# Kernel optimization log

Hardware: AMD Instinct MI355X
Metric: run time of the kernel (lower is better)

Reference implementation:

```python
import jax, jax.numpy as jnp
import numpy as np

EMBED, HEADS, LEVELS, POINTS = 256, 8, 3, 4
SPATIAL = np.array([[128, 128], [64, 64], [32, 32]], dtype=np.int64)  # (H, W) per level
B = 2
S = int((SPATIAL[:, 0] * SPATIAL[:, 1]).sum())  # 21504
Q = S  # encoder self-attention: queries == flattened multi-scale features


def grid_sample_bilinear(img, grid):
    """img: [N,C,H,W]; grid: [N,Q,P,2] (x,y) in [-1,1]; bilinear, zeros padding, align_corners=False.
    Returns [N,C,Q,P]."""
    N, C, H, W = img.shape
    _, Qn, Pn, _ = grid.shape
    x = (grid[..., 0] + 1.0) * (W * 0.5) - 0.5
    y = (grid[..., 1] + 1.0) * (H * 0.5) - 0.5
    x0 = jnp.floor(x)
    y0 = jnp.floor(y)
    wx1 = x - x0
    wy1 = y - y0
    x0i = x0.astype(jnp.int32)
    y0i = y0.astype(jnp.int32)
    imgf = img.reshape(N, C, H * W)

    def gather(ix, iy):
        valid = (ix >= 0) & (ix < W) & (iy >= 0) & (iy < H)
        ixc = jnp.clip(ix, 0, W - 1)
        iyc = jnp.clip(iy, 0, H - 1)
        flat = (iyc * W + ixc).reshape(N, -1)  # [N, Q*P]
        v = jax.vmap(lambda im, f: im[:, f])(imgf, flat)  # [N, C, Q*P]
        return jnp.where(valid.reshape(N, 1, -1), v, 0.0)

    w00 = ((1.0 - wx1) * (1.0 - wy1)).reshape(N, 1, -1)
    w01 = (wx1 * (1.0 - wy1)).reshape(N, 1, -1)
    w10 = ((1.0 - wx1) * wy1).reshape(N, 1, -1)
    w11 = (wx1 * wy1).reshape(N, 1, -1)
    out = (gather(x0i, y0i) * w00 + gather(x0i + 1, y0i) * w01
           + gather(x0i, y0i + 1) * w10 + gather(x0i + 1, y0i + 1) * w11)
    return out.reshape(N, C, Qn, Pn)


def msda_forward(hidden_states, encoder_hidden_states, reference_points, shapes_np,
                 sampling_offsets_w, sampling_offsets_b, attention_weights_w, attention_weights_b,
                 value_proj_w, value_proj_b, output_proj_w, output_proj_b):
    Bn, Qn, E = hidden_states.shape
    H, L, P = HEADS, LEVELS, POINTS
    D = E // H
    Sn = encoder_hidden_states.shape[1]
    value = (encoder_hidden_states @ value_proj_w.T + value_proj_b).reshape(Bn, Sn, H, D)
    off = (hidden_states @ sampling_offsets_w.T + sampling_offsets_b).reshape(Bn, Qn, H, L, P, 2)
    aw = hidden_states @ attention_weights_w.T + attention_weights_b
    aw = jax.nn.softmax(aw.reshape(Bn, Qn, H, L * P), axis=-1).reshape(Bn, Qn, H, L, P)
    # offset normalizer is (W, H) per level
    norm = jnp.asarray(np.stack([shapes_np[:, 1], shapes_np[:, 0]], axis=-1), dtype=hidden_states.dtype)
    loc = reference_points[:, :, None, :, None, :] + off / norm[None, None, None, :, None, :]
    grids = 2.0 * loc - 1.0  # [B,Q,H,L,P,2]
    out = jnp.zeros((Bn * H, D, Qn), value.dtype)
    start = 0
    for lvl in range(L):  # small static loop over levels (distinct spatial shapes)
        h, w = int(shapes_np[lvl, 0]), int(shapes_np[lvl, 1])
        val_l = value[:, start:start + h * w].transpose(0, 2, 3, 1).reshape(Bn * H, D, h, w)
        start += h * w
        g = grids[:, :, :, lvl].transpose(0, 2, 1, 3, 4).reshape(Bn * H, Qn, P, 2)
        sampled = grid_sample_bilinear(val_l, g)  # [B*H, D, Q, P]
        w_l = aw[:, :, :, lvl].transpose(0, 2, 1, 3).reshape(Bn * H, 1, Qn, P)
        out = out + (sampled * w_l).sum(-1)
    out = out.reshape(Bn, H * D, Qn).transpose(0, 2, 1)  # [B,Q,E]
    return out @ output_proj_w.T + output_proj_b


def setup_inputs():
    key = jax.random.key(0)
    ks = jax.random.split(key, 11)
    sc = 0.02
    E, H, L, P = EMBED, HEADS, LEVELS, POINTS
    return {
        "hidden_states": jax.random.normal(ks[0], (B, Q, E), jnp.float32),
        "encoder_hidden_states": jax.random.normal(ks[1], (B, S, E), jnp.float32),
        "reference_points": jax.random.uniform(ks[2], (B, Q, L, 2), jnp.float32),
        "spatial_shapes": jnp.asarray(SPATIAL),
        "sampling_offsets_w": jax.random.normal(ks[3], (H * L * P * 2, E), jnp.float32) * sc,
        "sampling_offsets_b": jax.random.normal(ks[4], (H * L * P * 2,), jnp.float32) * sc,
        "attention_weights_w": jax.random.normal(ks[5], (H * L * P, E), jnp.float32) * sc,
        "attention_weights_b": jax.random.normal(ks[6], (H * L * P,), jnp.float32) * sc,
        "value_proj_w": jax.random.normal(ks[7], (E, E), jnp.float32) * sc,
        "value_proj_b": jax.random.normal(ks[8], (E,), jnp.float32) * sc,
        "output_proj_w": jax.random.normal(ks[9], (E, E), jnp.float32) * sc,
        "output_proj_b": jax.random.normal(ks[10], (E,), jnp.float32) * sc,
    }


def reference(hidden_states, encoder_hidden_states, reference_points, spatial_shapes,
              sampling_offsets_w, sampling_offsets_b, attention_weights_w, attention_weights_b,
              value_proj_w, value_proj_b, output_proj_w, output_proj_b):
    shapes_np = np.asarray(spatial_shapes)  # static per-level (H, W)
    return msda_forward(hidden_states, encoder_hidden_states, reference_points, shapes_np,
                        sampling_offsets_w, sampling_offsets_b, attention_weights_w, attention_weights_b,
                        value_proj_w, value_proj_b, output_proj_w, output_proj_b)
```

## Files before the change

### kernel.cpp

```cpp
#include <hip/hip_runtime.h>
#include <hip/hip_bf16.h>

#define EMBED   256
#define HEADS   8
#define LEVELS  3
#define POINTS  4
#define BATCH   2
#define QLEN    21504
#define SLEN    21504
#define MTOT    (BATCH * QLEN)

typedef __attribute__((ext_vector_type(8))) short short8;
typedef __attribute__((ext_vector_type(4))) float f32x4;
typedef __attribute__((ext_vector_type(2))) float f32x2;

__device__ __forceinline__ short f2bf(float x) {
    unsigned u = __builtin_bit_cast(unsigned, x);
    u += 0x7fffu + ((u >> 16) & 1u);
    return (short)(u >> 16);
}
__device__ __forceinline__ f32x2 bfpair(unsigned u) {
    f32x2 r;
    r.x = __builtin_bit_cast(float, u << 16);
    r.y = __builtin_bit_cast(float, u & 0xffff0000u);
    return r;
}

__global__ __launch_bounds__(256)
void pack_weights_kernel(const float* __restrict__ vW, const float* __restrict__ oW,
                         const float* __restrict__ soW, const float* __restrict__ awW,
                         const float* __restrict__ soB, const float* __restrict__ awB,
                         short* __restrict__ vWf, short* __restrict__ oWf,
                         short* __restrict__ soawWf, float* __restrict__ soawB)
{
    int i = blockIdx.x * 256 + threadIdx.x;
    if (i < 25600) {
        const float* src; short* dst; int rem;
        if (i < 8192)       { src = vW; dst = vWf; rem = i; }
        else if (i < 16384) { src = oW; dst = oWf; rem = i - 8192; }
        else                { src = nullptr; dst = soawWf; rem = i - 16384; }
        const int lane = rem & 63;
        const int kt   = (rem >> 6) & 7;
        const int ct   = rem >> 9;
        const int col  = ct * 16 + (lane & 15);
        const int kb   = (kt * 4 + (lane >> 4)) * 8;
        const float* p = src ? (src + col * 256 + kb)
                             : ((col < 192) ? (soW + col * 256 + kb)
                                            : (awW + (col - 192) * 256 + kb));
        short8 t;
        #pragma unroll
        for (int j = 0; j < 8; ++j) t[j] = f2bf(p[j]);
        *(short8*)(dst + (size_t)rem * 8) = t;
    } else if (i < 25888) {
        int row = i - 25600;
        soawB[row] = (row < 192) ? soB[row] : awB[row - 192];
    }
}


__global__ __launch_bounds__(64, 4)
void proj_gemm_kernel(const float* __restrict__ enc, const short* __restrict__ vWf,
                      const float* __restrict__ vB, short* __restrict__ valb,
                      const float* __restrict__ hs, const short* __restrict__ soawWf,
                      const float* __restrict__ soawB, float* __restrict__ offaw)
{
    const int lane = threadIdx.x;
    const int m16  = lane & 15, ko = lane >> 4;
    const bool isVal = (blockIdx.x == 0);
    const float* A   = isVal ? enc : hs;
    const int strip  = blockIdx.y * 16;

    short8 afr[8];
    const float* Af = A + (size_t)(strip + m16) * 256 + ko * 8;
    #pragma unroll
    for (int kt = 0; kt < 8; ++kt) {
        float4 x = *(const float4*)(Af + kt * 32);
        float4 y = *(const float4*)(Af + kt * 32 + 4);
        short8 t;
        t[0] = f2bf(x.x); t[1] = f2bf(x.y); t[2] = f2bf(x.z); t[3] = f2bf(x.w);
        t[4] = f2bf(y.x); t[5] = f2bf(y.y); t[6] = f2bf(y.z); t[7] = f2bf(y.w);
        afr[kt] = t;
    }

    const short8* Wf  = (const short8*)(isVal ? vWf : soawWf);
    const float* bias = isVal ? vB : soawB;
    const int nct     = isVal ? 16 : 18;
    const int r0      = strip + ko * 4;

    for (int ct = 0; ct < nct; ++ct) {
        f32x4 a0 = (f32x4)0.f;
        #pragma unroll
        for (int kt = 0; kt < 8; ++kt) {
            const short8 bfrag = Wf[(ct * 8 + kt) * 64 + lane];
            a0 = __builtin_amdgcn_mfma_f32_16x16x32_bf16(afr[kt], bfrag, a0, 0, 0, 0);
        }
        const int col = ct * 16 + m16;
        const float bv = bias[col];
        if (isVal) {
            const int hh = col >> 5, ch = col & 31;
            #pragma unroll
            for (int r = 0; r < 4; ++r) {
                const int rg = r0 + r;
                const int b  = (rg >= SLEN) ? 1 : 0;
                const int sx = rg - b * SLEN;
                valb[(((size_t)(b * 8 + hh)) * SLEN + sx) * 32 + ch] = f2bf(a0[r] + bv);
            }
        } else {
            #pragma unroll
            for (int r = 0; r < 4; ++r)
                offaw[(size_t)(r0 + r) * 288 + col] = a0[r] + bv;
        }
    }
}

__global__ __launch_bounds__(64, 4)
void out_gemm_kernel(const short* __restrict__ A, const short* __restrict__ oWf,
                     const float* __restrict__ oB, float* __restrict__ C)
{
    const int lane = threadIdx.x;
    const int m16  = lane & 15, ko = lane >> 4;
    const int strip = blockIdx.x * 16;

    short8 afr[8];
    const short* Ab = A + (size_t)(strip + m16) * 256 + ko * 8;
    #pragma unroll
    for (int kt = 0; kt < 8; ++kt) afr[kt] = *(const short8*)(Ab + kt * 32);

    const short8* Wf = (const short8*)oWf;
    const int r0 = strip + ko * 4;
    for (int ct = 0; ct < 16; ++ct) {
        f32x4 a0 = (f32x4)0.f;
        #pragma unroll
        for (int kt = 0; kt < 8; ++kt) {
            const short8 bfrag = Wf[(ct * 8 + kt) * 64 + lane];
            a0 = __builtin_amdgcn_mfma_f32_16x16x32_bf16(afr[kt], bfrag, a0, 0, 0, 0);
        }
        const int col = ct * 16 + m16;
        const float bv = oB[col];
        #pragma unroll
        for (int r = 0; r < 4; ++r)
            C[(size_t)(r0 + r) * 256 + col] = a0[r] + bv;
    }
}

__global__ __launch_bounds__(256, 8)
void msda_sample_kernel(const short* __restrict__ value,
                        const float* __restrict__ offaw,
                        const float* __restrict__ ref,
                        short* __restrict__ attn)
{
    __shared__ int prep[32 * 76];

    const int tid = threadIdx.x;
    const int g   = tid >> 3;
    const int sub = tid & 7;
    const int t   = sub >> 2;

    const int blk = blockIdx.x;
    const int h   = blk & 7;
    const int j   = blk >> 3;
    const int b   = (j >= 672) ? 1 : 0;
    const int qc  = j - b * 672;
    const int q   = qc * 32 + g;
    const int bq  = b * QLEN + q;

    {
        const float* awp = offaw + (size_t)bq * 288 + 192 + h * 12;
        const float4 wa = *(const float4*)(awp);
        const float4 wb = *(const float4*)(awp + 4);
        const float4 wc = *(const float4*)(awp + 8);
        float w[12] = { wa.x, wa.y, wa.z, wa.w, wb.x, wb.y, wb.z, wb.w,
                        wc.x, wc.y, wc.z, wc.w };
        float mx = w[0];
        #pragma unroll
        for (int i = 1; i < 12; ++i) mx = fmaxf(mx, w[i]);
        float s = 0.f;
        #pragma unroll
        for (int i = 0; i < 12; ++i) s += __expf(w[i] - mx);
        const float inv = 1.f / s;

        const float* offp = offaw + (size_t)bq * 288 + h * 24;
        const float* refp = ref + (size_t)bq * 6;
        const int npts = (sub < 4) ? 2 : 1;
        #pragma unroll
        for (int it = 0; it < 2; ++it) {
            if (it >= npts) break;
            const int p  = sub + it * 8;
            const int l  = p >> 2;
            const int Wl = 128 >> l;
            const int st = (l == 0) ? 0 : (l == 1 ? 16384 : 20480);

            const float2 oxy = *(const float2*)(offp + p * 2);
            const float2 rxy = *(const float2*)(refp + 2 * l);
            const float ox = oxy.x, oy = oxy.y;
            const float rx = rxy.x, ry = rxy.y;
            const float a  = __expf(w[p] - mx) * inv;

            const float x = fmaf(rx, (float)Wl, ox - 0.5f);
            const float y = fmaf(ry, (float)Wl, oy - 0.5f);
            const float x0f = floorf(x), y0f = floorf(y);
            const int   x0  = (int)x0f,  y0  = (int)y0f;
            const float wx1 = x - x0f, wy1 = y - y0f;
            const float wx0 = 1.f - wx1, wy0 = 1.f - wy1;
            const bool vy0 = (unsigned)y0       < (unsigned)Wl;
            const bool vy1 = (unsigned)(y0 + 1) < (unsigned)Wl;

            const int xs = min(max(x0, 0), Wl - 2);
            const float wl0 = (xs == x0) ? wx0 : ((xs == x0 + 1) ? wx1 : 0.f);
            const float wl1 = (xs == x0) ? wx1 : ((xs + 1 == x0) ? wx0 : 0.f);

            const int hb = (b * 8 + h) * SLEN + st;
            const int o0 = vy0 ? (hb + y0 * Wl + xs) * 64       : 0;
            const int o1 = vy1 ? (hb + (y0 + 1) * Wl + xs) * 64 : 0;

            int* pp = &prep[g * 76 + p * 6];
            pp[0] = o0;
            pp[1] = o1;
            pp[2] = __builtin_bit_cast(int, vy0 ? wy0 * wl0 * a : 0.f);
            pp[3] = __builtin_bit_cast(int, vy0 ? wy0 * wl1 * a : 0.f);
            pp[4] = __builtin_bit_cast(int, vy1 ? wy1 * wl0 * a : 0.f);
            pp[5] = __builtin_bit_cast(int, vy1 ? wy1 * wl1 * a : 0.f);
        }
    }
    __syncthreads();

    const char* vbytes = (const char*)value;
    const unsigned subb = (unsigned)sub * 16u;
    f32x2 acc2[4];
    acc2[0] = (f32x2)0.f; acc2[1] = (f32x2)0.f;
    acc2[2] = (f32x2)0.f; acc2[3] = (f32x2)0.f;

    #pragma unroll
    for (int pb = 0; pb < 4; ++pb) {
        int4  v[6];
        float wgt[6];
        #pragma unroll
        for (int i = 0; i < 3; ++i) {
            const int p = pb * 3 + i;
            const int* pp = &prep[g * 76 + p * 6];
            const unsigned o0 = (unsigned)pp[0] + subb;
            const unsigned o1 = (unsigned)pp[1] + subb;
            wgt[2*i]   = __builtin_bit_cast(float, pp[2 + t]);
            wgt[2*i+1] = __builtin_bit_cast(float, pp[4 + t]);
            v[2*i]   = *(const int4*)(vbytes + (size_t)o0);
            v[2*i+1] = *(const int4*)(vbytes + (size_t)o1);
        }
        #pragma unroll
        for (int i = 0; i < 6; ++i) {
            f32x2 w2; w2.x = wgt[i]; w2.y = wgt[i];
            acc2[0] = __builtin_elementwise_fma(w2, bfpair((unsigned)v[i].x), acc2[0]);
            acc2[1] = __builtin_elementwise_fma(w2, bfpair((unsigned)v[i].y), acc2[1]);
            acc2[2] = __builtin_elementwise_fma(w2, bfpair((unsigned)v[i].z), acc2[2]);
            acc2[3] = __builtin_elementwise_fma(w2, bfpair((unsigned)v[i].w), acc2[3]);
        }
    }

    #pragma unroll
    for (int j2 = 0; j2 < 4; ++j2) {
        acc2[j2].x += __shfl_xor(acc2[j2].x, 4);
        acc2[j2].y += __shfl_xor(acc2[j2].y, 4);
    }

    if (sub < 4) {
        int4 o;
        o.x = ((unsigned)(unsigned short)f2bf(acc2[0].y) << 16) | (unsigned short)f2bf(acc2[0].x);
        o.y = ((unsigned)(unsigned short)f2bf(acc2[1].y) << 16) | (unsigned short)f2bf(acc2[1].x);
        o.z = ((unsigned)(unsigned short)f2bf(acc2[2].y) << 16) | (unsigned short)f2bf(acc2[2].x);
        o.w = ((unsigned)(unsigned short)f2bf(acc2[3].y) << 16) | (unsigned short)f2bf(acc2[3].x);
        ((int4*)attn)[(size_t)bq * 32 + h * 4 + sub] = o;
    }
}

extern "C" void kernel_launch(void* const* d_in, const int* in_sizes, int n_in,
                              void* d_out, int out_size, void* d_ws, size_t ws_size,
                              hipStream_t stream) {
    const float* hs  = (const float*)d_in[0];
    const float* enc = (const float*)d_in[1];
    const float* rp  = (const float*)d_in[2];
    const float* soW = (const float*)d_in[4];
    const float* soB = (const float*)d_in[5];
    const float* awW = (const float*)d_in[6];
    const float* awB = (const float*)d_in[7];
    const float* vW  = (const float*)d_in[8];
    const float* vB  = (const float*)d_in[9];
    const float* oW  = (const float*)d_in[10];
    const float* oB  = (const float*)d_in[11];
    float* out = (float*)d_out;

    const int M = MTOT;
    const size_t ME = (size_t)M * 256;

    short* valb   = (short*)d_ws;
    short* attnb  = valb + ME;
    float* offaw  = (float*)(attnb + ME);
    short* vWf    = (short*)(offaw + (size_t)M * 288);
    short* oWf    = vWf + 65536;
    short* soawWf = oWf + 65536;
    float* soawB  = (float*)(soawWf + 73728);

    pack_weights_kernel<<<dim3(102), dim3(256), 0, stream>>>(vW, oW, soW, awW, soB, awB,
                                                             vWf, oWf, soawWf, soawB);
    proj_gemm_kernel<<<dim3(2, M / 16), dim3(64), 0, stream>>>(enc, vWf, vB, valb,
                                                               hs, soawWf, soawB, offaw);
    msda_sample_kernel<<<dim3(M / 4), dim3(256), 0, stream>>>(valb, offaw, rp, attnb);
    out_gemm_kernel<<<dim3(M / 16), dim3(64), 0, stream>>>(attnb, oWf, oB, out);
}
```

Before: 270.2 us.

## Fuse all four stages into one persistent cooperative kernel with grid syncs

Merges the weight packing, projection GEMMs, deformable sampling and output GEMM into a single persistent cooperative kernel. The stages are separated by grid-wide syncs and work is spread with grid-stride loops over waves and blocks. The aim is to remove three kernel launch gaps and the tail effects between them. In exchange it adds grid barrier cost, caps the grid at 1024 blocks of 256 threads, and changes occupancy: the sampling stage moves from 8 to 4 blocks per CU and the GEMM stages from 64-thread blocks to 4 waves per block.

```diff
diff --git a/kernel.cpp b/kernel.cpp
--- a/kernel.cpp
+++ b/kernel.cpp
@@ -1,5 +1,8 @@
 #include <hip/hip_runtime.h>
 #include <hip/hip_bf16.h>
+#include <hip/hip_cooperative_groups.h>
+
+namespace cg = cooperative_groups;
 
 #define EMBED   256
 #define HEADS   8
@@ -26,248 +29,251 @@
     return r;
 }
 
-__global__ __launch_bounds__(256)
-void pack_weights_kernel(const float* __restrict__ vW, const float* __restrict__ oW,
-                         const float* __restrict__ soW, const float* __restrict__ awW,
-                         const float* __restrict__ soB, const float* __restrict__ awB,
-                         short* __restrict__ vWf, short* __restrict__ oWf,
-                         short* __restrict__ soawWf, float* __restrict__ soawB)
+__global__ __launch_bounds__(256, 4)
+void msda_fused(const float* __restrict__ hs, const float* __restrict__ enc,
+                const float* __restrict__ rp,
+                const float* __restrict__ soW, const float* __restrict__ soB,
+                const float* __restrict__ awW, const float* __restrict__ awB,
+                const float* __restrict__ vW,  const float* __restrict__ vB,
+                const float* __restrict__ oW,  const float* __restrict__ oB,
+                float* __restrict__ out,
+                short* __restrict__ valb, short* __restrict__ attnb,
+                float* __restrict__ offaw,
+                short* __restrict__ vWf, short* __restrict__ oWf,
+                short* __restrict__ soawWf, float* __restrict__ soawB)
 {
-    int i = blockIdx.x * 256 + threadIdx.x;
-    if (i < 25600) {
-        const float* src; short* dst; int rem;
-        if (i < 8192)       { src = vW; dst = vWf; rem = i; }
-        else if (i < 16384) { src = oW; dst = oWf; rem = i - 8192; }
-        else                { src = nullptr; dst = soawWf; rem = i - 16384; }
-        const int lane = rem & 63;
-        const int kt   = (rem >> 6) & 7;
-        const int ct   = rem >> 9;
-        const int col  = ct * 16 + (lane & 15);
-        const int kb   = (kt * 4 + (lane >> 4)) * 8;
-        const float* p = src ? (src + col * 256 + kb)
-                             : ((col < 192) ? (soW + col * 256 + kb)
-                                            : (awW + (col - 192) * 256 + kb));
-        short8 t;
-        #pragma unroll
-        for (int j = 0; j < 8; ++j) t[j] = f2bf(p[j]);
-        *(short8*)(dst + (size_t)rem * 8) = t;
-    } else if (i < 25888) {
-        int row = i - 25600;
-        soawB[row] = (row < 192) ? soB[row] : awB[row - 192];
-    }
-}
-
-
-__global__ __launch_bounds__(64, 4)
-void proj_gemm_kernel(const float* __restrict__ enc, const short* __restrict__ vWf,
-                      const float* __restrict__ vB, short* __restrict__ valb,
-                      const float* __restrict__ hs, const short* __restrict__ soawWf,
-                      const float* __restrict__ soawB, float* __restrict__ offaw)
-{
-    const int lane = threadIdx.x;
-    const int m16  = lane & 15, ko = lane >> 4;
-    const bool isVal = (blockIdx.x == 0);
-    const float* A   = isVal ? enc : hs;
-    const int strip  = blockIdx.y * 16;
-
-    short8 afr[8];
-    const float* Af = A + (size_t)(strip + m16) * 256 + ko * 8;
-    #pragma unroll
-    for (int kt = 0; kt < 8; ++kt) {
-        float4 x = *(const float4*)(Af + kt * 32);
-        float4 y = *(const float4*)(Af + kt * 32 + 4);
-        short8 t;
-        t[0] = f2bf(x.x); t[1] = f2bf(x.y); t[2] = f2bf(x.z); t[3] = f2bf(x.w);
-        t[4] = f2bf(y.x); t[5] = f2bf(y.y); t[6] = f2bf(y.z); t[7] = f2bf(y.w);
-        afr[kt] = t;
-    }
-
-    const short8* Wf  = (const short8*)(isVal ? vWf : soawWf);
-    const float* bias = isVal ? vB : soawB;
-    const int nct     = isVal ? 16 : 18;
-    const int r0      = strip + ko * 4;
-
-    for (int ct = 0; ct < nct; ++ct) {
-        f32x4 a0 = (f32x4)0.f;
+    __shared__ int prep[32 * 76];
+    cg::grid_group grid = cg::this_grid();
+
+    const int tid   = threadIdx.x;
+    const int nblk  = gridDim.x;
+    const int nwave = nblk * 4;
+    const int gwave = blockIdx.x * 4 + (tid >> 6);
+    const int lane  = tid & 63;
+    const int m16   = lane & 15, ko = lane >> 4;
+
+    for (int i = blockIdx.x * 256 + tid; i < 25888; i += nblk * 256) {
+        if (i < 25600) {
+            const float* src; short* dst; int rem;
+            if (i < 8192)       { src = vW; dst = vWf; rem = i; }
+            else if (i < 16384) { src = oW; dst = oWf; rem = i - 8192; }
+            else                { src = nullptr; dst = soawWf; rem = i - 16384; }
+            const int pl  = rem & 63;
+            const int kt  = (rem >> 6) & 7;
+            const int ct  = rem >> 9;
+            const int col = ct * 16 + (pl & 15);
+            const int kb  = (kt * 4 + (pl >> 4)) * 8;
+            const float* p = src ? (src + col * 256 + kb)
+                                 : ((col < 192) ? (soW + col * 256 + kb)
+                                                : (awW + (col - 192) * 256 + kb));
+            short8 t;
+            #pragma unroll
+            for (int j = 0; j < 8; ++j) t[j] = f2bf(p[j]);
+            *(short8*)(dst + (size_t)rem * 8) = t;
+        } else {
+            int row = i - 25600;
+            soawB[row] = (row < 192) ? soB[row] : awB[row - 192];
+        }
+    }
+    __threadfence();
+    grid.sync();
+
+    for (int u = gwave; u < 5376; u += nwave) {
+        const bool isVal = (u < 2688);
+        const int strip  = (isVal ? u : u - 2688) * 16;
+        const float* A   = isVal ? enc : hs;
+
+        short8 afr[8];
+        const float* Af = A + (size_t)(strip + m16) * 256 + ko * 8;
         #pragma unroll
         for (int kt = 0; kt < 8; ++kt) {
-            const short8 bfrag = Wf[(ct * 8 + kt) * 64 + lane];
-            a0 = __builtin_amdgcn_mfma_f32_16x16x32_bf16(afr[kt], bfrag, a0, 0, 0, 0);
-        }
-        const int col = ct * 16 + m16;
-        const float bv = bias[col];
-        if (isVal) {
-            const int hh = col >> 5, ch = col & 31;
-            #pragma unroll
-            for (int r = 0; r < 4; ++r) {
-                const int rg = r0 + r;
-                const int b  = (rg >= SLEN) ? 1 : 0;
-                const int sx = rg - b * SLEN;
-                valb[(((size_t)(b * 8 + hh)) * SLEN + sx) * 32 + ch] = f2bf(a0[r] + bv);
-            }
-        } else {
+            float4 x = *(const float4*)(Af + kt * 32);
+            float4 y = *(const float4*)(Af + kt * 32 + 4);
+            short8 t;
+            t[0] = f2bf(x.x); t[1] = f2bf(x.y); t[2] = f2bf(x.z); t[3] = f2bf(x.w);
+            t[4] = f2bf(y.x); t[5] = f2bf(y.y); t[6] = f2bf(y.z); t[7] = f2bf(y.w);
+            afr[kt] = t;
+        }
+
+        const short8* Wf  = (const short8*)(isVal ? vWf : soawWf);
+        const float* bias = isVal ? vB : soawB;
+        const int nct     = isVal ? 16 : 18;
+        const int r0      = strip + ko * 4;
+
+        for (int ct = 0; ct < nct; ++ct) {
+            f32x4 a0 = (f32x4)0.f;
+            #pragma unroll
+            for (int kt = 0; kt < 8; ++kt) {
+                const short8 bfrag = Wf[(ct * 8 + kt) * 64 + lane];
+                a0 = __builtin_amdgcn_mfma_f32_16x16x32_bf16(afr[kt], bfrag, a0, 0, 0, 0);
+            }
+            const int col = ct * 16 + m16;
+            const float bv = bias[col];
+            if (isVal) {
+                const int hh = col >> 5, ch = col & 31;
+                #pragma unroll
+                for (int r = 0; r < 4; ++r) {
+                    const int rg = r0 + r;
+                    const int b  = (rg >= SLEN) ? 1 : 0;
+                    const int sx = rg - b * SLEN;
+                    valb[(((size_t)(b * 8 + hh)) * SLEN + sx) * 32 + ch] = f2bf(a0[r] + bv);
+                }
+            } else {
+                #pragma unroll
+                for (int r = 0; r < 4; ++r)
+                    offaw[(size_t)(r0 + r) * 288 + col] = a0[r] + bv;
+            }
+        }
+    }
+    __threadfence();
+    grid.sync();
+
+    {
+        const int g   = tid >> 3;
+        const int sub = tid & 7;
+        const int t   = sub >> 2;
+
+        for (int u = blockIdx.x; u < 10752; u += nblk) {
+            const int h  = u & 7;
+            const int j  = u >> 3;
+            const int b  = (j >= 672) ? 1 : 0;
+            const int qc = j - b * 672;
+            const int q  = qc * 32 + g;
+            const int bq = b * QLEN + q;
+
+            {
+                const float* awp = offaw + (size_t)bq * 288 + 192 + h * 12;
+                const float4 wa = *(const float4*)(awp);
+                const float4 wb = *(const float4*)(awp + 4);
+                const float4 wc = *(const float4*)(awp + 8);
+                float w[12] = { wa.x, wa.y, wa.z, wa.w, wb.x, wb.y, wb.z, wb.w,
+                                wc.x, wc.y, wc.z, wc.w };
+                float mx = w[0];
+                #pragma unroll
+                for (int i = 1; i < 12; ++i) mx = fmaxf(mx, w[i]);
+                float s = 0.f;
+                #pragma unroll
+                for (int i = 0; i < 12; ++i) s += __expf(w[i] - mx);
+                const float inv = 1.f / s;
+
+                const float* offp = offaw + (size_t)bq * 288 + h * 24;
+                const float* refp = rp + (size_t)bq * 6;
+                const int npts = (sub < 4) ? 2 : 1;
+                #pragma unroll
+                for (int it = 0; it < 2; ++it) {
+                    if (it >= npts) break;
+                    const int p  = sub + it * 8;
+                    const int l  = p >> 2;
+                    const int Wl = 128 >> l;
+                    const int st = (l == 0) ? 0 : (l == 1 ? 16384 : 20480);
+
+                    const float2 oxy = *(const float2*)(offp + p * 2);
+                    const float2 rxy = *(const float2*)(refp + 2 * l);
+                    const float ox = oxy.x, oy = oxy.y;
+                    const float rx = rxy.x, ry = rxy.y;
+                    const float a  = __expf(w[p] - mx) * inv;
+
+                    const float x = fmaf(rx, (float)Wl, ox - 0.5f);
+                    const float y = fmaf(ry, (float)Wl, oy - 0.5f);
+                    const float x0f = floorf(x), y0f = floorf(y);
+                    const int   x0  = (int)x0f,  y0  = (int)y0f;
+                    const float wx1 = x - x0f, wy1 = y - y0f;
+                    const float wx0 = 1.f - wx1, wy0 = 1.f - wy1;
+                    const bool vy0 = (unsigned)y0       < (unsigned)Wl;
+                    const bool vy1 = (unsigned)(y0 + 1) < (unsigned)Wl;
+
+                    const int xs = min(max(x0, 0), Wl - 2);
+                    const float wl0 = (xs == x0) ? wx0 : ((xs == x0 + 1) ? wx1 : 0.f);
+                    const float wl1 = (xs == x0) ? wx1 : ((xs + 1 == x0) ? wx0 : 0.f);
+
+                    const int hb = (b * 8 + h) * SLEN + st;
+                    const int o0 = vy0 ? (hb + y0 * Wl + xs) * 64       : 0;
+                    const int o1 = vy1 ? (hb + (y0 + 1) * Wl + xs) * 64 : 0;
+
+                    int* pp = &prep[g * 76 + p * 6];
+                    pp[0] = o0;
+                    pp[1] = o1;
+                    pp[2] = __builtin_bit_cast(int, vy0 ? wy0 * wl0 * a : 0.f);
+                    pp[3] = __builtin_bit_cast(int, vy0 ? wy0 * wl1 * a : 0.f);
+                    pp[4] = __builtin_bit_cast(int, vy1 ? wy1 * wl0 * a : 0.f);
+                    pp[5] = __builtin_bit_cast(int, vy1 ? wy1 * wl1 * a : 0.f);
+                }
+            }
+            __syncthreads();
+
+            const char* vbytes = (const char*)valb;
+            const unsigned subb = (unsigned)sub * 16u;
+            f32x2 acc2[4];
+            acc2[0] = (f32x2)0.f; acc2[1] = (f32x2)0.f;
+            acc2[2] = (f32x2)0.f; acc2[3] = (f32x2)0.f;
+
+            #pragma unroll
+            for (int pb = 0; pb < 4; ++pb) {
+                int4  v[6];
+                float wgt[6];
+                #pragma unroll
+                for (int i = 0; i < 3; ++i) {
+                    const int p = pb * 3 + i;
+                    const int* pp = &prep[g * 76 + p * 6];
+                    const unsigned o0 = (unsigned)pp[0] + subb;
+                    const unsigned o1 = (unsigned)pp[1] + subb;
+                    wgt[2*i]   = __builtin_bit_cast(float, pp[2 + t]);
+                    wgt[2*i+1] = __builtin_bit_cast(float, pp[4 + t]);
+                    v[2*i]   = *(const int4*)(vbytes + (size_t)o0);
+                    v[2*i+1] = *(const int4*)(vbytes + (size_t)o1);
+                }
+                #pragma unroll
+                for (int i = 0; i < 6; ++i) {
+                    f32x2 w2; w2.x = wgt[i]; w2.y = wgt[i];
+                    acc2[0] = __builtin_elementwise_fma(w2, bfpair((unsigned)v[i].x), acc2[0]);
+                    acc2[1] = __builtin_elementwise_fma(w2, bfpair((unsigned)v[i].y), acc2[1]);
+                    acc2[2] = __builtin_elementwise_fma(w2, bfpair((unsigned)v[i].z), acc2[2]);
+                    acc2[3] = __builtin_elementwise_fma(w2, bfpair((unsigned)v[i].w), acc2[3]);
+                }
+            }
+
+            #pragma unroll
+            for (int j2 = 0; j2 < 4; ++j2) {
+                acc2[j2].x += __shfl_xor(acc2[j2].x, 4);
+                acc2[j2].y += __shfl_xor(acc2[j2].y, 4);
+            }
+
+            if (sub < 4) {
+                int4 o;
+                o.x = ((unsigned)(unsigned short)f2bf(acc2[0].y) << 16) | (unsigned short)f2bf(acc2[0].x);
+                o.y = ((unsigned)(unsigned short)f2bf(acc2[1].y) << 16) | (unsigned short)f2bf(acc2[1].x);
+                o.z = ((unsigned)(unsigned short)f2bf(acc2[2].y) << 16) | (unsigned short)f2bf(acc2[2].x);
+                o.w = ((unsigned)(unsigned short)f2bf(acc2[3].y) << 16) | (unsigned short)f2bf(acc2[3].x);
+                ((int4*)attnb)[(size_t)bq * 32 + h * 4 + sub] = o;
+            }
+            __syncthreads();
+        }
+    }
+    __threadfence();
+    grid.sync();
+
+    for (int u = gwave; u < 2688; u += nwave) {
+        const int strip = u * 16;
+        short8 afr[8];
+        const short* Ab = attnb + (size_t)(strip + m16) * 256 + ko * 8;
+        #pragma unroll
+        for (int kt = 0; kt < 8; ++kt) afr[kt] = *(const short8*)(Ab + kt * 32);
+
+        const short8* Wf = (const short8*)oWf;
+        const int r0 = strip + ko * 4;
+        for (int ct = 0; ct < 16; ++ct) {
+            f32x4 a0 = (f32x4)0.f;
+            #pragma unroll
+            for (int kt = 0; kt < 8; ++kt) {
+                const short8 bfrag = Wf[(ct * 8 + kt) * 64 + lane];
+                a0 = __builtin_amdgcn_mfma_f32_16x16x32_bf16(afr[kt], bfrag, a0, 0, 0, 0);
+            }
+            const int col = ct * 16 + m16;
+            const float bv = oB[col];
             #pragma unroll
             for (int r = 0; r < 4; ++r)
-                offaw[(size_t)(r0 + r) * 288 + col] = a0[r] + bv;
-        }
-    }
-}
-
-__global__ __launch_bounds__(64, 4)
-void out_gemm_kernel(const short* __restrict__ A, const short* __restrict__ oWf,
-                     const float* __restrict__ oB, float* __restrict__ C)
-{
-    const int lane = threadIdx.x;
-    const int m16  = lane & 15, ko = lane >> 4;
-    const int strip = blockIdx.x * 16;
-
-    short8 afr[8];
-    const short* Ab = A + (size_t)(strip + m16) * 256 + ko * 8;
-    #pragma unroll
-    for (int kt = 0; kt < 8; ++kt) afr[kt] = *(const short8*)(Ab + kt * 32);
-
-    const short8* Wf = (const short8*)oWf;
-    const int r0 = strip + ko * 4;
-    for (int ct = 0; ct < 16; ++ct) {
-        f32x4 a0 = (f32x4)0.f;
-        #pragma unroll
-        for (int kt = 0; kt < 8; ++kt) {
-            const short8 bfrag = Wf[(ct * 8 + kt) * 64 + lane];
-            a0 = __builtin_amdgcn_mfma_f32_16x16x32_bf16(afr[kt], bfrag, a0, 0, 0, 0);
-        }
-        const int col = ct * 16 + m16;
-        const float bv = oB[col];
-        #pragma unroll
-        for (int r = 0; r < 4; ++r)
-            C[(size_t)(r0 + r) * 256 + col] = a0[r] + bv;
-    }
-}
-
-__global__ __launch_bounds__(256, 8)
-void msda_sample_kernel(const short* __restrict__ value,
-                        const float* __restrict__ offaw,
-                        const float* __restrict__ ref,
-                        short* __restrict__ attn)
-{
-    __shared__ int prep[32 * 76];
-
-    const int tid = threadIdx.x;
-    const int g   = tid >> 3;
-    const int sub = tid & 7;
-    const int t   = sub >> 2;
-
-    const int blk = blockIdx.x;
-    const int h   = blk & 7;
-    const int j   = blk >> 3;
-    const int b   = (j >= 672) ? 1 : 0;
-    const int qc  = j - b * 672;
-    const int q   = qc * 32 + g;
-    const int bq  = b * QLEN + q;
-
-    {
-        const float* awp = offaw + (size_t)bq * 288 + 192 + h * 12;
-        const float4 wa = *(const float4*)(awp);
-        const float4 wb = *(const float4*)(awp + 4);
-        const float4 wc = *(const float4*)(awp + 8);
-        float w[12] = { wa.x, wa.y, wa.z, wa.w, wb.x, wb.y, wb.z, wb.w,
-                        wc.x, wc.y, wc.z, wc.w };
-        float mx = w[0];
-        #pragma unroll
-        for (int i = 1; i < 12; ++i) mx = fmaxf(mx, w[i]);
-        float s = 0.f;
-        #pragma unroll
-        for (int i = 0; i < 12; ++i) s += __expf(w[i] - mx);
-        const float inv = 1.f / s;
-
-        const float* offp = offaw + (size_t)bq * 288 + h * 24;
-        const float* refp = ref + (size_t)bq * 6;
-        const int npts = (sub < 4) ? 2 : 1;
-        #pragma unroll
-        for (int it = 0; it < 2; ++it) {
-            if (it >= npts) break;
-            const int p  = sub + it * 8;
-            const int l  = p >> 2;
-            const int Wl = 128 >> l;
-            const int st = (l == 0) ? 0 : (l == 1 ? 16384 : 20480);
-
-            const float2 oxy = *(const float2*)(offp + p * 2);
-            const float2 rxy = *(const float2*)(refp + 2 * l);
-            const float ox = oxy.x, oy = oxy.y;
-            const float rx = rxy.x, ry = rxy.y;
-            const float a  = __expf(w[p] - mx) * inv;
-
-            const float x = fmaf(rx, (float)Wl, ox - 0.5f);
-            const float y = fmaf(ry, (float)Wl, oy - 0.5f);
-            const float x0f = floorf(x), y0f = floorf(y);
-            const int   x0  = (int)x0f,  y0  = (int)y0f;
-            const float wx1 = x - x0f, wy1 = y - y0f;
-            const float wx0 = 1.f - wx1, wy0 = 1.f - wy1;
-            const bool vy0 = (unsigned)y0       < (unsigned)Wl;
-            const bool vy1 = (unsigned)(y0 + 1) < (unsigned)Wl;
-
-            const int xs = min(max(x0, 0), Wl - 2);
-            const float wl0 = (xs == x0) ? wx0 : ((xs == x0 + 1) ? wx1 : 0.f);
-            const float wl1 = (xs == x0) ? wx1 : ((xs + 1 == x0) ? wx0 : 0.f);
-
-            const int hb = (b * 8 + h) * SLEN + st;
-            const int o0 = vy0 ? (hb + y0 * Wl + xs) * 64       : 0;
-            const int o1 = vy1 ? (hb + (y0 + 1) * Wl + xs) * 64 : 0;
-
-            int* pp = &prep[g * 76 + p * 6];
-            pp[0] = o0;
-            pp[1] = o1;
-            pp[2] = __builtin_bit_cast(int, vy0 ? wy0 * wl0 * a : 0.f);
-            pp[3] = __builtin_bit_cast(int, vy0 ? wy0 * wl1 * a : 0.f);
-            pp[4] = __builtin_bit_cast(int, vy1 ? wy1 * wl0 * a : 0.f);
-            pp[5] = __builtin_bit_cast(int, vy1 ? wy1 * wl1 * a : 0.f);
-        }
-    }
-    __syncthreads();
-
-    const char* vbytes = (const char*)value;
-    const unsigned subb = (unsigned)sub * 16u;
-    f32x2 acc2[4];
-    acc2[0] = (f32x2)0.f; acc2[1] = (f32x2)0.f;
-    acc2[2] = (f32x2)0.f; acc2[3] = (f32x2)0.f;
-
-    #pragma unroll
-    for (int pb = 0; pb < 4; ++pb) {
-        int4  v[6];
-        float wgt[6];
-        #pragma unroll
-        for (int i = 0; i < 3; ++i) {
-            const int p = pb * 3 + i;
-            const int* pp = &prep[g * 76 + p * 6];
-            const unsigned o0 = (unsigned)pp[0] + subb;
-            const unsigned o1 = (unsigned)pp[1] + subb;
-            wgt[2*i]   = __builtin_bit_cast(float, pp[2 + t]);
-            wgt[2*i+1] = __builtin_bit_cast(float, pp[4 + t]);
-            v[2*i]   = *(const int4*)(vbytes + (size_t)o0);
-            v[2*i+1] = *(const int4*)(vbytes + (size_t)o1);
-        }
-        #pragma unroll
-        for (int i = 0; i < 6; ++i) {
-            f32x2 w2; w2.x = wgt[i]; w2.y = wgt[i];
-            acc2[0] = __builtin_elementwise_fma(w2, bfpair((unsigned)v[i].x), acc2[0]);
-            acc2[1] = __builtin_elementwise_fma(w2, bfpair((unsigned)v[i].y), acc2[1]);
-            acc2[2] = __builtin_elementwise_fma(w2, bfpair((unsigned)v[i].z), acc2[2]);
-            acc2[3] = __builtin_elementwise_fma(w2, bfpair((unsigned)v[i].w), acc2[3]);
-        }
-    }
-
-    #pragma unroll
-    for (int j2 = 0; j2 < 4; ++j2) {
-        acc2[j2].x += __shfl_xor(acc2[j2].x, 4);
-        acc2[j2].y += __shfl_xor(acc2[j2].y, 4);
-    }
-
-    if (sub < 4) {
-        int4 o;
-        o.x = ((unsigned)(unsigned short)f2bf(acc2[0].y) << 16) | (unsigned short)f2bf(acc2[0].x);
-        o.y = ((unsigned)(unsigned short)f2bf(acc2[1].y) << 16) | (unsigned short)f2bf(acc2[1].x);
-        o.z = ((unsigned)(unsigned short)f2bf(acc2[2].y) << 16) | (unsigned short)f2bf(acc2[2].x);
-        o.w = ((unsigned)(unsigned short)f2bf(acc2[3].y) << 16) | (unsigned short)f2bf(acc2[3].x);
-        ((int4*)attn)[(size_t)bq * 32 + h * 4 + sub] = o;
+                out[(size_t)(r0 + r) * 256 + col] = a0[r] + bv;
+        }
     }
 }
 
@@ -298,10 +304,22 @@
     short* soawWf = oWf + 65536;
     float* soawB  = (float*)(soawWf + 73728);
 
-    pack_weights_kernel<<<dim3(102), dim3(256), 0, stream>>>(vW, oW, soW, awW, soB, awB,
-                                                             vWf, oWf, soawWf, soawB);
-    proj_gemm_kernel<<<dim3(2, M / 16), dim3(64), 0, stream>>>(enc, vWf, vB, valb,
-                                                               hs, soawWf, soawB, offaw);
-    msda_sample_kernel<<<dim3(M / 4), dim3(256), 0, stream>>>(valb, offaw, rp, attnb);
-    out_gemm_kernel<<<dim3(M / 16), dim3(64), 0, stream>>>(attnb, oWf, oB, out);
+    static int maxBlk = -1;
+    if (maxBlk < 0) {
+        hipOccupancyMaxActiveBlocksPerMultiprocessor(&maxBlk, msda_fused, 256, 0);
+        if (maxBlk < 1) maxBlk = 1;
+    }
+    int grid = maxBlk * 256;
+    if (grid > 1024) grid = 1024;
+    grid = (grid / 8) * 8;
+    if (grid < 8) grid = 8;
+
+    void* args[] = { (void*)&hs, (void*)&enc, (void*)&rp,
+                     (void*)&soW, (void*)&soB, (void*)&awW, (void*)&awB,
+                     (void*)&vW, (void*)&vB, (void*)&oW, (void*)&oB,
+                     (void*)&out,
+                     (void*)&valb, (void*)&attnb, (void*)&offaw,
+                     (void*)&vWf, (void*)&oWf, (void*)&soawWf, (void*)&soawB };
+    hipLaunchCooperativeKernel((const void*)msda_fused, dim3(grid), dim3(256),
+                               args, 0, stream);
 }
```

New measurement: 646.5 us. +139.3%, slower.
